# Kernel optimization log

Hardware: AMD Instinct MI355X
Metric: run time of the kernel (lower is better)

The kernel has to match this reference:

```python
import jax, jax.numpy as jnp
import numpy as np
import math

D_KEY = 64
SCALE = math.sqrt(D_KEY)
INF = 1e10  # finite stand-in for the original INF constant
CAUSAL = True
DIAG = False


def setup_inputs() -> dict:
    key = jax.random.key(0)
    kq, kk, kv = jax.random.split(key, 3)
    B, L, D = 16, 2048, D_KEY
    return {
        "query": jax.random.normal(kq, (B, L, D), dtype=jnp.float32),
        "key": jax.random.normal(kk, (B, L, D), dtype=jnp.float32),
        "value": jax.random.normal(kv, (B, L, D), dtype=jnp.float32),
    }


def reference(query, key, value):
    # scores: [B, Lq, Lk]
    scores = jnp.einsum("bqd,bkd->bqk", query, key)
    L = key.shape[1]
    if CAUSAL:
        # subtract INF above the diagonal (strict upper triangle), as in torch triu(1)
        tri = jnp.triu(jnp.full((L, L), INF, dtype=scores.dtype), k=1)
        scores = scores - tri[None, :, :]
    if DIAG:
        # original scatters -INF onto the diagonal along dim 1
        diag_mask = jnp.eye(L, dtype=bool)
        scores = jnp.where(diag_mask[None, :, :], -INF, scores)
    # softmax over keys after scaling; dropout with p=0.0 is identity
    attn = jax.nn.softmax(scores / SCALE, axis=-1)
    return jnp.einsum("bqk,bkd->bqd", attn, value)
```

## Files before the change

kernel.cpp:

```cpp
#include <hip/hip_runtime.h>

typedef __bf16 bf16_t;
typedef __bf16 bf16x4 __attribute__((ext_vector_type(4)));
typedef __bf16 bf16x8 __attribute__((ext_vector_type(8)));
typedef float  f32x4  __attribute__((ext_vector_type(4)));

#define B_SZ  16
#define L_SEQ 2048
#define D_H   64
#define QB    64
#define KB    128
#define NQT   (L_SEQ / QB)

#define QSCALE 0.18033688011112043f

__global__ __launch_bounds__(512, 4)
void attn_pc_kernel(const float* __restrict__ Qg, const float* __restrict__ Kg,
                    const float* __restrict__ Vg, float* __restrict__ Og)
{
    const int lin  = blockIdx.x;
    const int xcd  = lin & 7;
    const int slot = lin >> 3;
    const int half = slot >> 5;
    const int qi   = slot & 31;
    const int b    = xcd * 2 + half;
    const int qt   = half ? qi : (31 - qi);

    const int tid  = threadIdx.x;
    const int wave = tid >> 6;
    const int lane = tid & 63;
    const int lg   = lane >> 4;
    const int lc   = lane & 15;

    __shared__ __align__(16) bf16_t K_lds[2][KB][72];
    __shared__ __align__(16) bf16_t Vt_lds[2][D_H][136];

    const size_t bbase = (size_t)b * L_SEQ * D_H;
    const int nkt = (qt + 2) >> 1;

    if (wave >= 4) {
        const int pt   = tid - 256;
        const int vkb  = pt & 31;
        const int vdg  = pt >> 5;
        const int vpos = ((vkb >> 3) << 5) + ((vkb & 3) << 3) + (((vkb >> 2) & 1) << 2);

        f32x4 kreg[8], vreg[8];

        auto issueK = [&](int kt) {
            const int kbase = kt * KB;
#pragma unroll
            for (int i = 0; i < 8; ++i) {
                const int f = i * 256 + pt;
                const int r = f >> 4, c4 = (f & 15) * 4;
                kreg[i] = *reinterpret_cast<const f32x4*>(Kg + bbase + (size_t)(kbase + r) * D_H + c4);
            }
        };
        auto issueV = [&](int kt) {
            const int kbase = kt * KB;
#pragma unroll
            for (int d2 = 0; d2 < 2; ++d2)
#pragma unroll
                for (int i = 0; i < 4; ++i)
                    vreg[d2 * 4 + i] = *reinterpret_cast<const f32x4*>(
                        Vg + bbase + (size_t)(kbase + vkb * 4 + i) * D_H + (vdg + d2 * 8) * 4);
        };
        auto writeK = [&](int buf) {
#pragma unroll
            for (int i = 0; i < 8; ++i) {
                const int f = i * 256 + pt;
                const int r = f >> 4, c4 = (f & 15) * 4;
                bf16x4 k4 = { (bf16_t)kreg[i][0], (bf16_t)kreg[i][1], (bf16_t)kreg[i][2], (bf16_t)kreg[i][3] };
                *reinterpret_cast<bf16x4*>(&K_lds[buf][r][c4]) = k4;
            }
        };
        auto writeV = [&](int buf) {
#pragma unroll
            for (int d2 = 0; d2 < 2; ++d2) {
                const int db = vdg + d2 * 8;
#pragma unroll
                for (int j = 0; j < 4; ++j) {
                    bf16x4 cj = { (bf16_t)vreg[d2 * 4 + 0][j], (bf16_t)vreg[d2 * 4 + 1][j],
                                  (bf16_t)vreg[d2 * 4 + 2][j], (bf16_t)vreg[d2 * 4 + 3][j] };
                    *reinterpret_cast<bf16x4*>(&Vt_lds[buf][db * 4 + j][vpos]) = cj;
                }
            }
        };

        issueK(0); issueV(0); writeK(0); writeV(0);
        __syncthreads();
        for (int kt = 0; kt < nkt; ++kt) {
            if (kt + 1 < nkt) {
                issueK(kt + 1); issueV(kt + 1);
                writeK((kt + 1) & 1); writeV((kt + 1) & 1);
            }
            __syncthreads();
        }
    } else {
        const int qrow = qt * QB + wave * 16 + lc;
        bf16x8 qa[2];
#pragma unroll
        for (int h = 0; h < 2; ++h) {
            const float* qp = Qg + bbase + (size_t)qrow * D_H + h * 32 + lg * 8;
            const f32x4 f0 = *reinterpret_cast<const f32x4*>(qp);
            const f32x4 f1 = *reinterpret_cast<const f32x4*>(qp + 4);
            bf16x8 a;
#pragma unroll
            for (int j = 0; j < 4; ++j) { a[j] = (bf16_t)(f0[j] * QSCALE); a[4 + j] = (bf16_t)(f1[j] * QSCALE); }
            qa[h] = a;
        }

        f32x4 o[4];
#pragma unroll
        for (int dt = 0; dt < 4; ++dt) o[dt] = (f32x4){0.f, 0.f, 0.f, 0.f};
        float m = -1e30f, l = 0.f;

        __syncthreads();
        for (int kt = 0; kt < nkt; ++kt) {
            const bool last = (kt == nkt - 1);
            const int kbase = kt * KB;
            const int cur   = kt & 1;

            f32x4 sc[8];
            __builtin_amdgcn_s_setprio(1);
#pragma unroll
            for (int n = 0; n < 8; ++n) {
                f32x4 acc = (f32x4){0.f, 0.f, 0.f, 0.f};
#pragma unroll
                for (int h = 0; h < 2; ++h) {
                    const bf16x8 kb = *reinterpret_cast<const bf16x8*>(&K_lds[cur][n * 16 + lc][h * 32 + lg * 8]);
                    acc = __builtin_amdgcn_mfma_f32_16x16x32_bf16(kb, qa[h], acc, 0, 0, 0);
                }
                sc[n] = acc;
            }
            __builtin_amdgcn_s_setprio(0);
            if (last) {
#pragma unroll
                for (int n = 0; n < 8; ++n)
#pragma unroll
                    for (int r = 0; r < 4; ++r)
                        if (kbase + n * 16 + lg * 4 + r > qrow) sc[n][r] = -1e30f;
            }

            float mxp = fmaxf(fmaxf(sc[0][0], sc[0][1]), fmaxf(sc[0][2], sc[0][3]));
#pragma unroll
            for (int n = 1; n < 8; ++n)
                mxp = fmaxf(mxp, fmaxf(fmaxf(sc[n][0], sc[n][1]), fmaxf(sc[n][2], sc[n][3])));
            if (!__all(mxp <= m + 8.0f)) {
                float mx = mxp;
                mx = fmaxf(mx, __shfl_xor(mx, 16));
                mx = fmaxf(mx, __shfl_xor(mx, 32));
                const float mn = fmaxf(m, mx);
                const float alpha = exp2f(m - mn);
                m = mn;
                l *= alpha;
#pragma unroll
                for (int dt = 0; dt < 4; ++dt)
#pragma unroll
                    for (int r = 0; r < 4; ++r) o[dt][r] *= alpha;
            }
            bf16x8 w[4];
            float rs = 0.f;
#pragma unroll
            for (int n = 0; n < 8; ++n) {
                const float p0 = exp2f(sc[n][0] - m), p1 = exp2f(sc[n][1] - m);
                const float p2 = exp2f(sc[n][2] - m), p3 = exp2f(sc[n][3] - m);
                rs += (p0 + p1) + (p2 + p3);
                const int wi = n >> 1, off = (n & 1) * 4;
                w[wi][off + 0] = (bf16_t)p0; w[wi][off + 1] = (bf16_t)p1;
                w[wi][off + 2] = (bf16_t)p2; w[wi][off + 3] = (bf16_t)p3;
            }
            l += rs;

            __builtin_amdgcn_s_setprio(1);
#pragma unroll
            for (int ks = 0; ks < 4; ++ks) {
#pragma unroll
                for (int dt = 0; dt < 4; ++dt) {
                    const bf16x8 vb = *reinterpret_cast<const bf16x8*>(&Vt_lds[cur][dt * 16 + lc][ks * 32 + lg * 8]);
                    o[dt] = __builtin_amdgcn_mfma_f32_16x16x32_bf16(vb, w[ks], o[dt], 0, 0, 0);
                }
            }
            __builtin_amdgcn_s_setprio(0);

            __syncthreads();
        }

        float lr = l;
        lr += __shfl_xor(lr, 16);
        lr += __shfl_xor(lr, 32);
        const float inv = 1.0f / lr;
#pragma unroll
        for (int dt = 0; dt < 4; ++dt) {
            f32x4 val = { o[dt][0] * inv, o[dt][1] * inv, o[dt][2] * inv, o[dt][3] * inv };
            *reinterpret_cast<f32x4*>(Og + bbase + (size_t)qrow * D_H + dt * 16 + lg * 4) = val;
        }
    }
}

extern "C" void kernel_launch(void* const* d_in, const int* in_sizes, int n_in,
                              void* d_out, int out_size, void* d_ws, size_t ws_size,
                              hipStream_t stream)
{
    const float* Q = (const float*)d_in[0];
    const float* K = (const float*)d_in[1];
    const float* V = (const float*)d_in[2];
    float* O = (float*)d_out;
    attn_pc_kernel<<<dim3(NQT * B_SZ), dim3(512), 0, stream>>>(Q, K, V, O);
}
```

Measured before the change: 33.92 us.

## Balance causal work by pairing query tiles and splitting KV with a merge kernel

Pairs each long query tile (31-p) with a short one (p) and splits the combined 17 KV tiles across two blocks of 9 and 8 tiles, so every block does nearly equal work instead of the triangular imbalance. The long tile's partial O, max and sum from the two blocks are written to workspace and combined by a second merge kernel. This targets the tail where blocks with many KV tiles dominate runtime. In exchange it adds an extra kernel launch, partial-result global traffic, and falls back to the old kernel when the workspace is too small.

```diff
diff --git a/kernel.cpp b/kernel.cpp
--- a/kernel.cpp
+++ b/kernel.cpp
@@ -10,9 +10,267 @@
 #define D_H   64
 #define QB    64
 #define KB    128
-#define NQT   (L_SEQ / QB)
 
 #define QSCALE 0.18033688011112043f
+
+#define OPART_FL ((size_t)512 * QB * D_H)
+#define ML_FL    ((size_t)512 * 128)
+
+__global__ __launch_bounds__(512, 4)
+void attn_pcs_kernel(const float* __restrict__ Qg, const float* __restrict__ Kg,
+                     const float* __restrict__ Vg, float* __restrict__ Og,
+                     float* __restrict__ Opart, float* __restrict__ MLb)
+{
+    const int lin  = blockIdx.x;
+    const int xcd  = lin & 7;
+    const int b    = xcd * 2 + ((lin >> 3) & 1);
+    const int p    = (lin >> 4) & 15;
+    const int role = lin >> 8;
+    const int pair = b * 16 + p;
+
+    const int nktL = (33 - p) >> 1;
+    const int cnt1 = role ? (nktL - 9) : 9;
+    const int total = role ? 8 : 9;
+
+    const int tid  = threadIdx.x;
+    const int wave = tid >> 6;
+    const int lane = tid & 63;
+    const int lg   = lane >> 4;
+    const int lc   = lane & 15;
+
+    __shared__ __align__(16) bf16_t K_lds[2][KB][72];
+    __shared__ __align__(16) bf16_t Vt_lds[2][D_H][136];
+
+    const size_t bbase = (size_t)b * L_SEQ * D_H;
+
+    auto seqKt = [&](int j) {
+        const int pos = role * 9 + j;
+        return pos < nktL ? pos : pos - nktL;
+    };
+
+    if (wave >= 4) {
+        const int pt   = tid - 256;
+        const int vkb  = pt & 31;
+        const int vdg  = pt >> 5;
+        const int vpos = ((vkb >> 3) << 5) + ((vkb & 3) << 3) + (((vkb >> 2) & 1) << 2);
+
+        f32x4 kreg[8], vreg[8];
+
+        auto issueK = [&](int kt) {
+            const int kbase = kt * KB;
+#pragma unroll
+            for (int i = 0; i < 8; ++i) {
+                const int f = i * 256 + pt;
+                const int r = f >> 4, c4 = (f & 15) * 4;
+                kreg[i] = *reinterpret_cast<const f32x4*>(Kg + bbase + (size_t)(kbase + r) * D_H + c4);
+            }
+        };
+        auto issueV = [&](int kt) {
+            const int kbase = kt * KB;
+#pragma unroll
+            for (int d2 = 0; d2 < 2; ++d2)
+#pragma unroll
+                for (int i = 0; i < 4; ++i)
+                    vreg[d2 * 4 + i] = *reinterpret_cast<const f32x4*>(
+                        Vg + bbase + (size_t)(kbase + vkb * 4 + i) * D_H + (vdg + d2 * 8) * 4);
+        };
+        auto writeK = [&](int buf) {
+#pragma unroll
+            for (int i = 0; i < 8; ++i) {
+                const int f = i * 256 + pt;
+                const int r = f >> 4, c4 = (f & 15) * 4;
+                bf16x4 k4 = { (bf16_t)kreg[i][0], (bf16_t)kreg[i][1], (bf16_t)kreg[i][2], (bf16_t)kreg[i][3] };
+                *reinterpret_cast<bf16x4*>(&K_lds[buf][r][c4]) = k4;
+            }
+        };
+        auto writeV = [&](int buf) {
+#pragma unroll
+            for (int d2 = 0; d2 < 2; ++d2) {
+                const int db = vdg + d2 * 8;
+#pragma unroll
+                for (int j = 0; j < 4; ++j) {
+                    bf16x4 cj = { (bf16_t)vreg[d2 * 4 + 0][j], (bf16_t)vreg[d2 * 4 + 1][j],
+                                  (bf16_t)vreg[d2 * 4 + 2][j], (bf16_t)vreg[d2 * 4 + 3][j] };
+                    *reinterpret_cast<bf16x4*>(&Vt_lds[buf][db * 4 + j][vpos]) = cj;
+                }
+            }
+        };
+
+        issueK(seqKt(0)); issueV(seqKt(0)); writeK(0); writeV(0);
+        __syncthreads();
+        for (int j = 0; j < total; ++j) {
+            if (j + 1 < total) {
+                const int nk = seqKt(j + 1);
+                issueK(nk); issueV(nk);
+                writeK((j + 1) & 1); writeV((j + 1) & 1);
+            }
+            __syncthreads();
+        }
+    } else {
+        bf16x8 qa[2];
+        int qrow;
+        auto loadQ = [&](int qt_) {
+            qrow = qt_ * QB + wave * 16 + lc;
+#pragma unroll
+            for (int h = 0; h < 2; ++h) {
+                const float* qp = Qg + bbase + (size_t)qrow * D_H + h * 32 + lg * 8;
+                const f32x4 f0 = *reinterpret_cast<const f32x4*>(qp);
+                const f32x4 f1 = *reinterpret_cast<const f32x4*>(qp + 4);
+                bf16x8 a;
+#pragma unroll
+                for (int j = 0; j < 4; ++j) { a[j] = (bf16_t)(f0[j] * QSCALE); a[4 + j] = (bf16_t)(f1[j] * QSCALE); }
+                qa[h] = a;
+            }
+        };
+
+        loadQ(31 - p);
+
+        f32x4 o[4];
+#pragma unroll
+        for (int dt = 0; dt < 4; ++dt) o[dt] = (f32x4){0.f, 0.f, 0.f, 0.f};
+        float m = -1e30f, l = 0.f;
+
+        auto writePartialL = [&]() {
+            float lr = l;
+            lr += __shfl_xor(lr, 16);
+            lr += __shfl_xor(lr, 32);
+            const int slot = pair * 2 + role;
+            float* ob = Opart + (size_t)slot * (QB * D_H);
+            const int qL = wave * 16 + lc;
+#pragma unroll
+            for (int dt = 0; dt < 4; ++dt)
+                *reinterpret_cast<f32x4*>(&ob[qL * 64 + dt * 16 + lg * 4]) = o[dt];
+            if (lg == 0) { MLb[slot * 128 + qL] = m; MLb[slot * 128 + 64 + qL] = lr; }
+        };
+
+        __syncthreads();
+        for (int j = 0; j < total; ++j) {
+            if (role && j == cnt1) {
+                writePartialL();
+                loadQ(p);
+#pragma unroll
+                for (int dt = 0; dt < 4; ++dt) o[dt] = (f32x4){0.f, 0.f, 0.f, 0.f};
+                m = -1e30f; l = 0.f;
+            }
+            const int pos = role * 9 + j;
+            const int kt  = pos < nktL ? pos : pos - nktL;
+            const int kb0 = kt * KB;
+            const int cur = j & 1;
+
+            f32x4 sc[8];
+            __builtin_amdgcn_s_setprio(1);
+#pragma unroll
+            for (int n = 0; n < 8; ++n) {
+                f32x4 acc = (f32x4){0.f, 0.f, 0.f, 0.f};
+#pragma unroll
+                for (int h = 0; h < 2; ++h) {
+                    const bf16x8 kb = *reinterpret_cast<const bf16x8*>(&K_lds[cur][n * 16 + lc][h * 32 + lg * 8]);
+                    acc = __builtin_amdgcn_mfma_f32_16x16x32_bf16(kb, qa[h], acc, 0, 0, 0);
+                }
+                sc[n] = acc;
+            }
+            __builtin_amdgcn_s_setprio(0);
+
+            const bool diag = (pos == nktL - 1) || (pos == 16);
+            if (diag) {
+#pragma unroll
+                for (int n = 0; n < 8; ++n)
+#pragma unroll
+                    for (int r = 0; r < 4; ++r)
+                        if (kb0 + n * 16 + lg * 4 + r > qrow) sc[n][r] = -1e30f;
+            }
+
+            float mxp = fmaxf(fmaxf(sc[0][0], sc[0][1]), fmaxf(sc[0][2], sc[0][3]));
+#pragma unroll
+            for (int n = 1; n < 8; ++n)
+                mxp = fmaxf(mxp, fmaxf(fmaxf(sc[n][0], sc[n][1]), fmaxf(sc[n][2], sc[n][3])));
+            if (!__all(mxp <= m + 8.0f)) {
+                float mx = mxp;
+                mx = fmaxf(mx, __shfl_xor(mx, 16));
+                mx = fmaxf(mx, __shfl_xor(mx, 32));
+                const float mn = fmaxf(m, mx);
+                const float alpha = exp2f(m - mn);
+                m = mn;
+                l *= alpha;
+#pragma unroll
+                for (int dt = 0; dt < 4; ++dt)
+#pragma unroll
+                    for (int r = 0; r < 4; ++r) o[dt][r] *= alpha;
+            }
+            bf16x8 w[4];
+            float rs = 0.f;
+#pragma unroll
+            for (int n = 0; n < 8; ++n) {
+                const float p0 = exp2f(sc[n][0] - m), p1 = exp2f(sc[n][1] - m);
+                const float p2 = exp2f(sc[n][2] - m), p3 = exp2f(sc[n][3] - m);
+                rs += (p0 + p1) + (p2 + p3);
+                const int wi = n >> 1, off = (n & 1) * 4;
+                w[wi][off + 0] = (bf16_t)p0; w[wi][off + 1] = (bf16_t)p1;
+                w[wi][off + 2] = (bf16_t)p2; w[wi][off + 3] = (bf16_t)p3;
+            }
+            l += rs;
+
+            __builtin_amdgcn_s_setprio(1);
+#pragma unroll
+            for (int ks = 0; ks < 4; ++ks) {
+#pragma unroll
+                for (int dt = 0; dt < 4; ++dt) {
+                    const bf16x8 vb = *reinterpret_cast<const bf16x8*>(&Vt_lds[cur][dt * 16 + lc][ks * 32 + lg * 8]);
+                    o[dt] = __builtin_amdgcn_mfma_f32_16x16x32_bf16(vb, w[ks], o[dt], 0, 0, 0);
+                }
+            }
+            __builtin_amdgcn_s_setprio(0);
+
+            __syncthreads();
+        }
+
+        if (role == 0) {
+            writePartialL();
+        } else {
+            float lr = l;
+            lr += __shfl_xor(lr, 16);
+            lr += __shfl_xor(lr, 32);
+            const float inv = 1.0f / lr;
+#pragma unroll
+            for (int dt = 0; dt < 4; ++dt) {
+                f32x4 val = { o[dt][0] * inv, o[dt][1] * inv, o[dt][2] * inv, o[dt][3] * inv };
+                *reinterpret_cast<f32x4*>(Og + bbase + (size_t)qrow * D_H + dt * 16 + lg * 4) = val;
+            }
+        }
+    }
+}
+
+__global__ __launch_bounds__(256)
+void merge_kernel(const float* __restrict__ Opart, const float* __restrict__ MLb,
+                  float* __restrict__ Og)
+{
+    const int pairIdx = blockIdx.x;
+    const int b  = pairIdx >> 4, p = pairIdx & 15;
+    const int qt = 31 - p;
+    const int t  = threadIdx.x;
+    const int q  = t >> 2;
+    const int dc = (t & 3) << 4;
+
+    const int slot0 = pairIdx * 2, slot1 = slot0 + 1;
+    const float m0 = MLb[slot0 * 128 + q], l0 = MLb[slot0 * 128 + 64 + q];
+    const float m1 = MLb[slot1 * 128 + q], l1 = MLb[slot1 * 128 + 64 + q];
+    const float mt = fmaxf(m0, m1);
+    const float a0 = exp2f(m0 - mt), a1 = exp2f(m1 - mt);
+    const float inv = 1.0f / (l0 * a0 + l1 * a1);
+
+    const float* o0 = Opart + (size_t)slot0 * (QB * D_H) + q * 64 + dc;
+    const float* o1 = Opart + (size_t)slot1 * (QB * D_H) + q * 64 + dc;
+    float* og = Og + (size_t)b * L_SEQ * D_H + (size_t)(qt * QB + q) * D_H + dc;
+#pragma unroll
+    for (int i = 0; i < 4; ++i) {
+        const f32x4 v0 = *reinterpret_cast<const f32x4*>(o0 + i * 4);
+        const f32x4 v1 = *reinterpret_cast<const f32x4*>(o1 + i * 4);
+        f32x4 r;
+#pragma unroll
+        for (int k = 0; k < 4; ++k) r[k] = (v0[k] * a0 + v1[k] * a1) * inv;
+        *reinterpret_cast<f32x4*>(og + i * 4) = r;
+    }
+}
 
 __global__ __launch_bounds__(512, 4)
 void attn_pc_kernel(const float* __restrict__ Qg, const float* __restrict__ Kg,
@@ -45,7 +303,6 @@
         const int vpos = ((vkb >> 3) << 5) + ((vkb & 3) << 3) + (((vkb >> 2) & 1) << 2);
 
         f32x4 kreg[8], vreg[8];
-
         auto issueK = [&](int kt) {
             const int kbase = kt * KB;
 #pragma unroll
@@ -108,7 +365,6 @@
             for (int j = 0; j < 4; ++j) { a[j] = (bf16_t)(f0[j] * QSCALE); a[4 + j] = (bf16_t)(f1[j] * QSCALE); }
             qa[h] = a;
         }
-
         f32x4 o[4];
 #pragma unroll
         for (int dt = 0; dt < 4; ++dt) o[dt] = (f32x4){0.f, 0.f, 0.f, 0.f};
@@ -119,7 +375,6 @@
             const bool last = (kt == nkt - 1);
             const int kbase = kt * KB;
             const int cur   = kt & 1;
-
             f32x4 sc[8];
             __builtin_amdgcn_s_setprio(1);
 #pragma unroll
@@ -140,7 +395,6 @@
                     for (int r = 0; r < 4; ++r)
                         if (kbase + n * 16 + lg * 4 + r > qrow) sc[n][r] = -1e30f;
             }
-
             float mxp = fmaxf(fmaxf(sc[0][0], sc[0][1]), fmaxf(sc[0][2], sc[0][3]));
 #pragma unroll
             for (int n = 1; n < 8; ++n)
@@ -151,8 +405,7 @@
                 mx = fmaxf(mx, __shfl_xor(mx, 32));
                 const float mn = fmaxf(m, mx);
                 const float alpha = exp2f(m - mn);
-                m = mn;
-                l *= alpha;
+                m = mn; l *= alpha;
 #pragma unroll
                 for (int dt = 0; dt < 4; ++dt)
 #pragma unroll
@@ -170,7 +423,6 @@
                 w[wi][off + 2] = (bf16_t)p2; w[wi][off + 3] = (bf16_t)p3;
             }
             l += rs;
-
             __builtin_amdgcn_s_setprio(1);
 #pragma unroll
             for (int ks = 0; ks < 4; ++ks) {
@@ -181,10 +433,8 @@
                 }
             }
             __builtin_amdgcn_s_setprio(0);
-
             __syncthreads();
         }
-
         float lr = l;
         lr += __shfl_xor(lr, 16);
         lr += __shfl_xor(lr, 32);
@@ -205,5 +455,14 @@
     const float* K = (const float*)d_in[1];
     const float* V = (const float*)d_in[2];
     float* O = (float*)d_out;
-    attn_pc_kernel<<<dim3(NQT * B_SZ), dim3(512), 0, stream>>>(Q, K, V, O);
+
+    const size_t need = (OPART_FL + ML_FL) * sizeof(float);
+    if (ws_size >= need) {
+        float* Opart = (float*)d_ws;
+        float* MLb   = Opart + OPART_FL;
+        attn_pcs_kernel<<<dim3(512), dim3(512), 0, stream>>>(Q, K, V, O, Opart, MLb);
+        merge_kernel<<<dim3(256), dim3(256), 0, stream>>>(Opart, MLb, O);
+    } else {
+        attn_pc_kernel<<<dim3(512), dim3(512), 0, stream>>>(Q, K, V, O);
+    }
 }
```

New measurement: 37.62 us. +10.9%, slower.

## Replace block-wide barriers with LDS counter flags between producer and consumer waves

Applied to the files above, without the earlier changes.

Swaps the per-tile __syncthreads between the loader waves and the compute waves for LDS counters: producers bump ready counters after writing a buffer, and consumers bump done counters after reading it. Each side polls with s_sleep, so producers and consumers can drift apart by up to the double-buffer depth instead of moving in lockstep. This risks spin-wait overhead and depends on correct LDS memory ordering through s_waitcnt, which is subtle. Producers now also issue global loads for tile j before waiting on the buffer to free.

```diff
diff --git a/kernel.cpp b/kernel.cpp
--- a/kernel.cpp
+++ b/kernel.cpp
@@ -15,8 +15,8 @@
 #define QSCALE 0.18033688011112043f
 
 __global__ __launch_bounds__(512, 4)
-void attn_pc_kernel(const float* __restrict__ Qg, const float* __restrict__ Kg,
-                    const float* __restrict__ Vg, float* __restrict__ Og)
+void attn_pcf_kernel(const float* __restrict__ Qg, const float* __restrict__ Kg,
+                     const float* __restrict__ Vg, float* __restrict__ Og)
 {
     const int lin  = blockIdx.x;
     const int xcd  = lin & 7;
@@ -34,9 +34,18 @@
 
     __shared__ __align__(16) bf16_t K_lds[2][KB][72];
     __shared__ __align__(16) bf16_t Vt_lds[2][D_H][136];
+    __shared__ int ready_cnt[2];
+    __shared__ int done_cnt[2];
+
+    if (tid == 0) { ready_cnt[0] = ready_cnt[1] = 0; done_cnt[0] = done_cnt[1] = 0; }
+    __syncthreads();
 
     const size_t bbase = (size_t)b * L_SEQ * D_H;
     const int nkt = (qt + 2) >> 1;
+
+    auto pollGE = [&](volatile int* p, int target) {
+        while (*p < target) __builtin_amdgcn_s_sleep(2);
+    };
 
     if (wave >= 4) {
         const int pt   = tid - 256;
@@ -86,14 +95,14 @@
             }
         };
 
-        issueK(0); issueV(0); writeK(0); writeV(0);
-        __syncthreads();
-        for (int kt = 0; kt < nkt; ++kt) {
-            if (kt + 1 < nkt) {
-                issueK(kt + 1); issueV(kt + 1);
-                writeK((kt + 1) & 1); writeV((kt + 1) & 1);
-            }
-            __syncthreads();
+        for (int j = 0; j < nkt; ++j) {
+            const int buf = j & 1;
+            issueK(j); issueV(j);
+            if (j >= 2) pollGE((volatile int*)&done_cnt[buf], 4 * (j >> 1));
+            writeK(buf); writeV(buf);
+            asm volatile("s_waitcnt lgkmcnt(0)" ::: "memory");
+            __builtin_amdgcn_sched_barrier(0);
+            if (lane == 0) atomicAdd(&ready_cnt[buf], 1);
         }
     } else {
         const int qrow = qt * QB + wave * 16 + lc;
@@ -114,11 +123,12 @@
         for (int dt = 0; dt < 4; ++dt) o[dt] = (f32x4){0.f, 0.f, 0.f, 0.f};
         float m = -1e30f, l = 0.f;
 
-        __syncthreads();
         for (int kt = 0; kt < nkt; ++kt) {
             const bool last = (kt == nkt - 1);
             const int kbase = kt * KB;
             const int cur   = kt & 1;
+
+            pollGE((volatile int*)&ready_cnt[cur], 4 * ((kt >> 1) + 1));
 
             f32x4 sc[8];
             __builtin_amdgcn_s_setprio(1);
@@ -182,7 +192,9 @@
             }
             __builtin_amdgcn_s_setprio(0);
 
-            __syncthreads();
+            asm volatile("s_waitcnt lgkmcnt(0)" ::: "memory");
+            __builtin_amdgcn_sched_barrier(0);
+            if (lane == 0) atomicAdd(&done_cnt[cur], 1);
         }
 
         float lr = l;
@@ -205,5 +217,5 @@
     const float* K = (const float*)d_in[1];
     const float* V = (const float*)d_in[2];
     float* O = (float*)d_out;
-    attn_pc_kernel<<<dim3(NQT * B_SZ), dim3(512), 0, stream>>>(Q, K, V, O);
+    attn_pcf_kernel<<<dim3(NQT * B_SZ), dim3(512), 0, stream>>>(Q, K, V, O);
 }
```

Measured after the change: 34.15 us. No clear change (+0.7%).

## Halve block to 256 threads, each compute wave handles two 16-row query groups

Applied to the files above, without the earlier changes.

Shrinks the workgroup from 8 waves (4 producers, 4 consumers) to 4 waves (2 producers, 2 consumers). Each consumer wave now processes 32 query rows as two 16-row groups, so every K and V fragment read from LDS feeds two MFMAs. Each producer thread stages twice as much K/V data. The aim is less LDS traffic per MFMA and fewer waves per block. The cost is more registers per thread, and the producers issue fewer loads in parallel, which may expose global load latency.

```diff
diff --git a/kernel.cpp b/kernel.cpp
--- a/kernel.cpp
+++ b/kernel.cpp
@@ -14,9 +14,9 @@
 
 #define QSCALE 0.18033688011112043f
 
-__global__ __launch_bounds__(512, 4)
-void attn_pc_kernel(const float* __restrict__ Qg, const float* __restrict__ Kg,
-                    const float* __restrict__ Vg, float* __restrict__ Og)
+__global__ __launch_bounds__(256, 2)
+void attn_pc2_kernel(const float* __restrict__ Qg, const float* __restrict__ Kg,
+                     const float* __restrict__ Vg, float* __restrict__ Og)
 {
     const int lin  = blockIdx.x;
     const int xcd  = lin & 7;
@@ -38,45 +38,43 @@
     const size_t bbase = (size_t)b * L_SEQ * D_H;
     const int nkt = (qt + 2) >> 1;
 
-    if (wave >= 4) {
-        const int pt   = tid - 256;
+    if (wave >= 2) {
+        const int pt   = tid - 128;
         const int vkb  = pt & 31;
-        const int vdg  = pt >> 5;
+        const int vdg2 = pt >> 5;
         const int vpos = ((vkb >> 3) << 5) + ((vkb & 3) << 3) + (((vkb >> 2) & 1) << 2);
 
-        f32x4 kreg[8], vreg[8];
-
-        auto issueK = [&](int kt) {
+        f32x4 kreg[16], vreg[16];
+
+        auto stageK = [&](int kt, int buf) {
             const int kbase = kt * KB;
 #pragma unroll
-            for (int i = 0; i < 8; ++i) {
-                const int f = i * 256 + pt;
+            for (int i = 0; i < 16; ++i) {
+                const int f = i * 128 + pt;
                 const int r = f >> 4, c4 = (f & 15) * 4;
                 kreg[i] = *reinterpret_cast<const f32x4*>(Kg + bbase + (size_t)(kbase + r) * D_H + c4);
             }
-        };
-        auto issueV = [&](int kt) {
-            const int kbase = kt * KB;
-#pragma unroll
-            for (int d2 = 0; d2 < 2; ++d2)
-#pragma unroll
-                for (int i = 0; i < 4; ++i)
-                    vreg[d2 * 4 + i] = *reinterpret_cast<const f32x4*>(
-                        Vg + bbase + (size_t)(kbase + vkb * 4 + i) * D_H + (vdg + d2 * 8) * 4);
-        };
-        auto writeK = [&](int buf) {
-#pragma unroll
-            for (int i = 0; i < 8; ++i) {
-                const int f = i * 256 + pt;
+#pragma unroll
+            for (int i = 0; i < 16; ++i) {
+                const int f = i * 128 + pt;
                 const int r = f >> 4, c4 = (f & 15) * 4;
                 bf16x4 k4 = { (bf16_t)kreg[i][0], (bf16_t)kreg[i][1], (bf16_t)kreg[i][2], (bf16_t)kreg[i][3] };
                 *reinterpret_cast<bf16x4*>(&K_lds[buf][r][c4]) = k4;
             }
         };
-        auto writeV = [&](int buf) {
-#pragma unroll
-            for (int d2 = 0; d2 < 2; ++d2) {
-                const int db = vdg + d2 * 8;
+        auto stageV = [&](int kt, int buf) {
+            const int kbase = kt * KB;
+#pragma unroll
+            for (int d2 = 0; d2 < 4; ++d2) {
+                const int db = vdg2 + d2 * 4;
+#pragma unroll
+                for (int i = 0; i < 4; ++i)
+                    vreg[d2 * 4 + i] = *reinterpret_cast<const f32x4*>(
+                        Vg + bbase + (size_t)(kbase + vkb * 4 + i) * D_H + db * 4);
+            }
+#pragma unroll
+            for (int d2 = 0; d2 < 4; ++d2) {
+                const int db = vdg2 + d2 * 4;
 #pragma unroll
                 for (int j = 0; j < 4; ++j) {
                     bf16x4 cj = { (bf16_t)vreg[d2 * 4 + 0][j], (bf16_t)vreg[d2 * 4 + 1][j],
@@ -86,33 +84,36 @@
             }
         };
 
-        issueK(0); issueV(0); writeK(0); writeV(0);
+        stageK(0, 0); stageV(0, 0);
         __syncthreads();
         for (int kt = 0; kt < nkt; ++kt) {
-            if (kt + 1 < nkt) {
-                issueK(kt + 1); issueV(kt + 1);
-                writeK((kt + 1) & 1); writeV((kt + 1) & 1);
-            }
+            if (kt + 1 < nkt) { stageK(kt + 1, (kt + 1) & 1); stageV(kt + 1, (kt + 1) & 1); }
             __syncthreads();
         }
     } else {
-        const int qrow = qt * QB + wave * 16 + lc;
-        bf16x8 qa[2];
-#pragma unroll
-        for (int h = 0; h < 2; ++h) {
-            const float* qp = Qg + bbase + (size_t)qrow * D_H + h * 32 + lg * 8;
-            const f32x4 f0 = *reinterpret_cast<const f32x4*>(qp);
-            const f32x4 f1 = *reinterpret_cast<const f32x4*>(qp + 4);
-            bf16x8 a;
-#pragma unroll
-            for (int j = 0; j < 4; ++j) { a[j] = (bf16_t)(f0[j] * QSCALE); a[4 + j] = (bf16_t)(f1[j] * QSCALE); }
-            qa[h] = a;
-        }
-
-        f32x4 o[4];
-#pragma unroll
-        for (int dt = 0; dt < 4; ++dt) o[dt] = (f32x4){0.f, 0.f, 0.f, 0.f};
-        float m = -1e30f, l = 0.f;
+        const int qrow0 = qt * QB + wave * 32 + lc;
+        bf16x8 qa[2][2];
+#pragma unroll
+        for (int g = 0; g < 2; ++g)
+#pragma unroll
+            for (int h = 0; h < 2; ++h) {
+                const float* qp = Qg + bbase + (size_t)(qrow0 + g * 16) * D_H + h * 32 + lg * 8;
+                const f32x4 f0 = *reinterpret_cast<const f32x4*>(qp);
+                const f32x4 f1 = *reinterpret_cast<const f32x4*>(qp + 4);
+                bf16x8 a;
+#pragma unroll
+                for (int j = 0; j < 4; ++j) { a[j] = (bf16_t)(f0[j] * QSCALE); a[4 + j] = (bf16_t)(f1[j] * QSCALE); }
+                qa[g][h] = a;
+            }
+
+        f32x4 o[2][4];
+        float m[2], l[2];
+#pragma unroll
+        for (int g = 0; g < 2; ++g) {
+#pragma unroll
+            for (int dt = 0; dt < 4; ++dt) o[g][dt] = (f32x4){0.f, 0.f, 0.f, 0.f};
+            m[g] = -1e30f; l[g] = 0.f;
+        }
 
         __syncthreads();
         for (int kt = 0; kt < nkt; ++kt) {
@@ -120,56 +121,65 @@
             const int kbase = kt * KB;
             const int cur   = kt & 1;
 
-            f32x4 sc[8];
+            f32x4 sc[2][8];
             __builtin_amdgcn_s_setprio(1);
 #pragma unroll
             for (int n = 0; n < 8; ++n) {
-                f32x4 acc = (f32x4){0.f, 0.f, 0.f, 0.f};
+                f32x4 a0 = (f32x4){0.f, 0.f, 0.f, 0.f};
+                f32x4 a1 = (f32x4){0.f, 0.f, 0.f, 0.f};
 #pragma unroll
                 for (int h = 0; h < 2; ++h) {
                     const bf16x8 kb = *reinterpret_cast<const bf16x8*>(&K_lds[cur][n * 16 + lc][h * 32 + lg * 8]);
-                    acc = __builtin_amdgcn_mfma_f32_16x16x32_bf16(kb, qa[h], acc, 0, 0, 0);
-                }
-                sc[n] = acc;
+                    a0 = __builtin_amdgcn_mfma_f32_16x16x32_bf16(kb, qa[0][h], a0, 0, 0, 0);
+                    a1 = __builtin_amdgcn_mfma_f32_16x16x32_bf16(kb, qa[1][h], a1, 0, 0, 0);
+                }
+                sc[0][n] = a0; sc[1][n] = a1;
             }
             __builtin_amdgcn_s_setprio(0);
             if (last) {
 #pragma unroll
-                for (int n = 0; n < 8; ++n)
-#pragma unroll
-                    for (int r = 0; r < 4; ++r)
-                        if (kbase + n * 16 + lg * 4 + r > qrow) sc[n][r] = -1e30f;
-            }
-
-            float mxp = fmaxf(fmaxf(sc[0][0], sc[0][1]), fmaxf(sc[0][2], sc[0][3]));
-#pragma unroll
-            for (int n = 1; n < 8; ++n)
-                mxp = fmaxf(mxp, fmaxf(fmaxf(sc[n][0], sc[n][1]), fmaxf(sc[n][2], sc[n][3])));
-            if (!__all(mxp <= m + 8.0f)) {
-                float mx = mxp;
-                mx = fmaxf(mx, __shfl_xor(mx, 16));
-                mx = fmaxf(mx, __shfl_xor(mx, 32));
-                const float mn = fmaxf(m, mx);
-                const float alpha = exp2f(m - mn);
-                m = mn;
-                l *= alpha;
-#pragma unroll
-                for (int dt = 0; dt < 4; ++dt)
-#pragma unroll
-                    for (int r = 0; r < 4; ++r) o[dt][r] *= alpha;
-            }
-            bf16x8 w[4];
-            float rs = 0.f;
-#pragma unroll
-            for (int n = 0; n < 8; ++n) {
-                const float p0 = exp2f(sc[n][0] - m), p1 = exp2f(sc[n][1] - m);
-                const float p2 = exp2f(sc[n][2] - m), p3 = exp2f(sc[n][3] - m);
-                rs += (p0 + p1) + (p2 + p3);
-                const int wi = n >> 1, off = (n & 1) * 4;
-                w[wi][off + 0] = (bf16_t)p0; w[wi][off + 1] = (bf16_t)p1;
-                w[wi][off + 2] = (bf16_t)p2; w[wi][off + 3] = (bf16_t)p3;
-            }
-            l += rs;
+                for (int g = 0; g < 2; ++g) {
+                    const int qr = qrow0 + g * 16;
+#pragma unroll
+                    for (int n = 0; n < 8; ++n)
+#pragma unroll
+                        for (int r = 0; r < 4; ++r)
+                            if (kbase + n * 16 + lg * 4 + r > qr) sc[g][n][r] = -1e30f;
+                }
+            }
+
+            bf16x8 w[2][4];
+#pragma unroll
+            for (int g = 0; g < 2; ++g) {
+                float mxp = fmaxf(fmaxf(sc[g][0][0], sc[g][0][1]), fmaxf(sc[g][0][2], sc[g][0][3]));
+#pragma unroll
+                for (int n = 1; n < 8; ++n)
+                    mxp = fmaxf(mxp, fmaxf(fmaxf(sc[g][n][0], sc[g][n][1]), fmaxf(sc[g][n][2], sc[g][n][3])));
+                if (!__all(mxp <= m[g] + 8.0f)) {
+                    float mx = mxp;
+                    mx = fmaxf(mx, __shfl_xor(mx, 16));
+                    mx = fmaxf(mx, __shfl_xor(mx, 32));
+                    const float mn = fmaxf(m[g], mx);
+                    const float alpha = exp2f(m[g] - mn);
+                    m[g] = mn;
+                    l[g] *= alpha;
+#pragma unroll
+                    for (int dt = 0; dt < 4; ++dt)
+#pragma unroll
+                        for (int r = 0; r < 4; ++r) o[g][dt][r] *= alpha;
+                }
+                float rs = 0.f;
+#pragma unroll
+                for (int n = 0; n < 8; ++n) {
+                    const float p0 = exp2f(sc[g][n][0] - m[g]), p1 = exp2f(sc[g][n][1] - m[g]);
+                    const float p2 = exp2f(sc[g][n][2] - m[g]), p3 = exp2f(sc[g][n][3] - m[g]);
+                    rs += (p0 + p1) + (p2 + p3);
+                    const int wi = n >> 1, off = (n & 1) * 4;
+                    w[g][wi][off + 0] = (bf16_t)p0; w[g][wi][off + 1] = (bf16_t)p1;
+                    w[g][wi][off + 2] = (bf16_t)p2; w[g][wi][off + 3] = (bf16_t)p3;
+                }
+                l[g] += rs;
+            }
 
             __builtin_amdgcn_s_setprio(1);
 #pragma unroll
@@ -177,7 +187,8 @@
 #pragma unroll
                 for (int dt = 0; dt < 4; ++dt) {
                     const bf16x8 vb = *reinterpret_cast<const bf16x8*>(&Vt_lds[cur][dt * 16 + lc][ks * 32 + lg * 8]);
-                    o[dt] = __builtin_amdgcn_mfma_f32_16x16x32_bf16(vb, w[ks], o[dt], 0, 0, 0);
+                    o[0][dt] = __builtin_amdgcn_mfma_f32_16x16x32_bf16(vb, w[0][ks], o[0][dt], 0, 0, 0);
+                    o[1][dt] = __builtin_amdgcn_mfma_f32_16x16x32_bf16(vb, w[1][ks], o[1][dt], 0, 0, 0);
                 }
             }
             __builtin_amdgcn_s_setprio(0);
@@ -185,14 +196,17 @@
             __syncthreads();
         }
 
-        float lr = l;
-        lr += __shfl_xor(lr, 16);
-        lr += __shfl_xor(lr, 32);
-        const float inv = 1.0f / lr;
-#pragma unroll
-        for (int dt = 0; dt < 4; ++dt) {
-            f32x4 val = { o[dt][0] * inv, o[dt][1] * inv, o[dt][2] * inv, o[dt][3] * inv };
-            *reinterpret_cast<f32x4*>(Og + bbase + (size_t)qrow * D_H + dt * 16 + lg * 4) = val;
+#pragma unroll
+        for (int g = 0; g < 2; ++g) {
+            float lr = l[g];
+            lr += __shfl_xor(lr, 16);
+            lr += __shfl_xor(lr, 32);
+            const float inv = 1.0f / lr;
+#pragma unroll
+            for (int dt = 0; dt < 4; ++dt) {
+                f32x4 val = { o[g][dt][0] * inv, o[g][dt][1] * inv, o[g][dt][2] * inv, o[g][dt][3] * inv };
+                *reinterpret_cast<f32x4*>(Og + bbase + (size_t)(qrow0 + g * 16) * D_H + dt * 16 + lg * 4) = val;
+            }
         }
     }
 }
@@ -205,5 +219,5 @@
     const float* K = (const float*)d_in[1];
     const float* V = (const float*)d_in[2];
     float* O = (float*)d_out;
-    attn_pc_kernel<<<dim3(NQT * B_SZ), dim3(512), 0, stream>>>(Q, K, V, O);
+    attn_pc2_kernel<<<dim3(NQT * B_SZ), dim3(256), 0, stream>>>(Q, K, V, O);
 }
```

Result: slower. 50.16 us (+47.9%).
